# Performance work log

Hardware: AMD Instinct MI355X
Metric: run time of the kernel (lower is better)

## Reference

```python
import jax, jax.numpy as jnp
import numpy as np

N = 100000
E = 1600000
IN_C, HID_C, OUT_C = 128, 64, 40


def setup_inputs() -> dict:
    key = jax.random.key(0)
    ks = jax.random.split(key, 9)
    x = jax.random.normal(ks[0], (N, IN_C), dtype=jnp.float32)
    src = jax.random.randint(ks[1], (E,), 0, N, dtype=jnp.int64)
    dst = jax.random.randint(ks[2], (E,), 0, N, dtype=jnp.int64)
    edge_index = jnp.stack([src, dst], axis=0)
    def glorot(k, fan_in, fan_out):
        s = jnp.sqrt(6.0 / (fan_in + fan_out)).astype(jnp.float32)
        return jax.random.uniform(k, (fan_in, fan_out), jnp.float32, -s, s)
    return {
        "x": x,
        "edge_index": edge_index,
        "W1": glorot(ks[3], IN_C, HID_C), "b1": jnp.zeros((HID_C,), jnp.float32),
        "W2": glorot(ks[4], HID_C, HID_C), "b2": jnp.zeros((HID_C,), jnp.float32),
        "W3": glorot(ks[5], HID_C, OUT_C), "b3": jnp.zeros((OUT_C,), jnp.float32),
    }


def _gcn_norm(edge_index, n_nodes):
    # add self-loops, then symmetric normalization D^-1/2 (A+I) D^-1/2
    loops = jnp.arange(n_nodes, dtype=edge_index.dtype)
    src = jnp.concatenate([edge_index[0], loops])
    dst = jnp.concatenate([edge_index[1], loops])
    deg = jax.ops.segment_sum(jnp.ones_like(dst, dtype=jnp.float32), dst,
                              num_segments=n_nodes)
    dinv = jnp.where(deg > 0, jax.lax.rsqrt(deg), 0.0)
    norm = dinv[src] * dinv[dst]  # [E + N]
    return src, dst, norm


def _gcn_conv(h, W, b, src, dst, norm, n_nodes):
    h = h @ W                                   # [N, out]
    msg = norm[:, None] * h[src]                # gather + scale, [E+N, out]
    out = jax.ops.segment_sum(msg, dst, num_segments=n_nodes)  # scatter-add
    return out + b


def reference(x, edge_index, W1, b1, W2, b2, W3, b3):
    n_nodes = x.shape[0]
    src, dst, norm = _gcn_norm(edge_index, n_nodes)
    h = jax.nn.relu(_gcn_conv(x, W1, b1, src, dst, norm, n_nodes))
    # dropout(p=0.5) is identity in eval mode
    h = jax.nn.relu(_gcn_conv(h, W2, b2, src, dst, norm, n_nodes))
    out = _gcn_conv(h, W3, b3, src, dst, norm, n_nodes)
    return out
```

## Files before the change

### kernel.cpp

```cpp
#include <hip/hip_runtime.h>

#define N_NODES 100000
#define N_EDGES 1600000
#define NBUCK 196
#define BCAP 9600
#define CH 4096
#define NCHUNK ((N_EDGES + CH - 1) / CH)
#define DBINS 64

typedef __attribute__((ext_vector_type(2))) _Float16 half2v;
typedef __attribute__((ext_vector_type(4))) _Float16 half4v;
typedef __attribute__((ext_vector_type(8))) _Float16 half8v;
typedef __attribute__((ext_vector_type(4))) float f32x4;

__device__ __forceinline__ float4 loadX4(const float* X, size_t idx) {
    return *(const float4*)(X + idx);
}
__device__ __forceinline__ float4 loadX4(const _Float16* X, size_t idx) {
    half4v h = *(const half4v*)(X + idx);
    return make_float4((float)h.x, (float)h.y, (float)h.z, (float)h.w);
}


__global__ __launch_bounds__(256) void zero_small(int* p, int n) {
    int i = blockIdx.x * blockDim.x + threadIdx.x;
    if (i < n) p[i] = 0;
}

__global__ __launch_bounds__(256) void multisplit(const int* __restrict__ src,
                                                  const int* __restrict__ dst,
                                                  int* cursor,
                                                  int* __restrict__ bucketed, int e) {
    __shared__ int cnt[NBUCK];
    __shared__ int basel[NBUCK];
    const int t = threadIdx.x;
    const int base_e = blockIdx.x * CH;

    int myS[16], myD[16];
    for (int i = t; i < NBUCK; i += 256) cnt[i] = 0;
    __syncthreads();

#pragma unroll
    for (int k = 0; k < 16; ++k) {
        int i = base_e + k * 256 + t;
        if (i < e) {
            myS[k] = src[i];
            myD[k] = dst[i];
            atomicAdd(&cnt[myD[k] >> 9], 1);
        } else {
            myD[k] = -1;
        }
    }
    __syncthreads();
    for (int i = t; i < NBUCK; i += 256) basel[i] = atomicAdd(&cursor[i], cnt[i]);
    __syncthreads();
    for (int i = t; i < NBUCK; i += 256) cnt[i] = 0;
    __syncthreads();

#pragma unroll
    for (int k = 0; k < 16; ++k) {
        if (myD[k] >= 0) {
            int b = myD[k] >> 9;
            int pos = basel[b] + atomicAdd(&cnt[b], 1);
            if (pos < BCAP)
                bucketed[(size_t)b * BCAP + pos] = ((myD[k] & 511) << 17) | myS[k];
        }
    }
}

__global__ __launch_bounds__(256) void bucket_scan(const int* __restrict__ cursor,
                                                   int* __restrict__ gbase) {
    __shared__ int sm[256];
    const int t = threadIdx.x;
    int v = (t < NBUCK) ? cursor[t] : 0;
    sm[t] = v;
    __syncthreads();
    for (int off = 1; off < 256; off <<= 1) {
        int u = (t >= off) ? sm[t - off] : 0;
        __syncthreads();
        sm[t] += u;
        __syncthreads();
    }
    if (t < NBUCK) gbase[t] = sm[t] - v;
    if (t == NBUCK - 1) gbase[NBUCK] = sm[t];
}

__global__ __launch_bounds__(512) void build_csr(const int* __restrict__ bucketed,
                                                 const int* __restrict__ gbase,
                                                 int* __restrict__ row_ptr,
                                                 float* __restrict__ dinv,
                                                 int* __restrict__ csr_src,
                                                 int* __restrict__ hist, int n) {
    __shared__ int vals[BCAP];
    __shared__ int cnt[512];
    __shared__ int lcur[512];
    __shared__ int lhist[DBINS];
    const int b = blockIdx.x;
    const int t = threadIdx.x;
    const int nb0 = b * 512;
    const int nn = min(512, n - nb0);
    const int gb = gbase[b];
    const int m = gbase[b + 1] - gb;

    cnt[t] = 0;
    if (t < DBINS) lhist[t] = 0;
    __syncthreads();
    for (int i = t; i < m; i += 512) {
        int v = bucketed[(size_t)b * BCAP + i];
        vals[i] = v;
        atomicAdd(&cnt[v >> 17], 1);
    }
    __syncthreads();

    int deg = cnt[t];
    if (t < nn) atomicAdd(&lhist[min(deg, DBINS - 1)], 1);
    for (int off = 1; off < 512; off <<= 1) {
        int u = (t >= off) ? cnt[t - off] : 0;
        __syncthreads();
        cnt[t] += u;
        __syncthreads();
    }
    int offv = cnt[t] - deg;
    __syncthreads();
    cnt[t] = offv;
    lcur[t] = 0;
    if (t < nn) {
        row_ptr[nb0 + t] = gb + offv;
        dinv[nb0 + t] = rsqrtf((float)(deg + 1));
    }
    if (b == NBUCK - 1 && t == 0) row_ptr[n] = gb + m;
    __syncthreads();

    for (int i = t; i < m; i += 512) {
        int v = vals[i];
        int node = v >> 17;
        int pos = atomicAdd(&lcur[node], 1);
        csr_src[gb + cnt[node] + pos] = v & 0x1FFFF;
    }
    if (t < DBINS && lhist[t] > 0) atomicAdd(&hist[t], lhist[t]);
}


__global__ __launch_bounds__(64) void hist_scan(const int* __restrict__ hist,
                                                int* __restrict__ base) {
    __shared__ int sm[DBINS];
    const int t = threadIdx.x;
    int v = hist[t];
    sm[t] = v;
    __syncthreads();
    for (int off = 1; off < DBINS; off <<= 1) {
        int u = (t >= off) ? sm[t - off] : 0;
        __syncthreads();
        sm[t] += u;
        __syncthreads();
    }
    base[t] = sm[t] - v;
}

__global__ __launch_bounds__(256) void perm_scatter(const int* __restrict__ row_ptr,
                                                    const int* __restrict__ base,
                                                    int* gcursor,
                                                    int* __restrict__ perm, int n) {
    __shared__ int lcnt[DBINS];
    __shared__ int lbase[DBINS];
    const int t = threadIdx.x;
    if (t < DBINS) lcnt[t] = 0;
    __syncthreads();
    const int i = blockIdx.x * 256 + t;
    int bin = 0, lpos = 0;
    if (i < n) {
        int deg = row_ptr[i + 1] - row_ptr[i];
        bin = min(deg, DBINS - 1);
        lpos = atomicAdd(&lcnt[bin], 1);
    }
    __syncthreads();
    if (t < DBINS && lcnt[t] > 0) lbase[t] = atomicAdd(&gcursor[t], lcnt[t]);
    __syncthreads();
    if (i < n) perm[base[bin] + lbase[bin] + lpos] = i;
}


template <int K>
__global__ __launch_bounds__(256) void transpose_w(const float* __restrict__ W,
                                                   _Float16* __restrict__ Wt) {
    int i = blockIdx.x * 256 + threadIdx.x;
    if (i < K * 64) {
        int k = i >> 6, nn = i & 63;
        Wt[(size_t)nn * K + k] = (_Float16)W[i];
    }
}


__device__ __forceinline__ void stageX_rows(const float* X, _Float16* Xl, int t,
                                            int row0, int n, int K, int SP) {
    for (int i = t; i < 64 * K / 4; i += 256) {
        int r = i / (K / 4), c = (i % (K / 4)) * 4;
        int grow = min(row0 + r, n - 1);
        float4 v = *(const float4*)(X + (size_t)grow * K + c);
        half4v h = {(_Float16)v.x, (_Float16)v.y, (_Float16)v.z, (_Float16)v.w};
        *(half4v*)(Xl + r * SP + c) = h;
    }
}
__device__ __forceinline__ void stageX_rows(const _Float16* X, _Float16* Xl, int t,
                                            int row0, int n, int K, int SP) {
    for (int i = t; i < 64 * K / 8; i += 256) {
        int r = i / (K / 8), c = (i % (K / 8)) * 8;
        int grow = min(row0 + r, n - 1);
        *(half8v*)(Xl + r * SP + c) = *(const half8v*)(X + (size_t)grow * K + c);
    }
}

template <int K, typename XT>
__global__ __launch_bounds__(256) void gemm_mfma64(const XT* __restrict__ X,
                                                   const _Float16* __restrict__ Wt,
                                                   const float* __restrict__ dinv,
                                                   _Float16* __restrict__ Y, int n) {
    constexpr int SP = K + 8;
    __shared__ _Float16 Xl[64 * SP];
    __shared__ _Float16 Wl[64 * SP];
    const int t = threadIdx.x;
    const int wave = t >> 6, lane = t & 63;
    const int row0 = blockIdx.x * 64;
    const int m = lane & 15, quad = lane >> 4;

    if (blockIdx.x == 0 && t < 32) ((int*)(Y + (size_t)n * 64))[t] = 0;

    for (int i = t; i < 64 * K / 8; i += 256) {
        int r = i / (K / 8), c = (i % (K / 8)) * 8;
        *(half8v*)(Wl + r * SP + c) = *(const half8v*)(Wt + (size_t)r * K + c);
    }
    stageX_rows(X, Xl, t, row0, n, K, SP);
    __syncthreads();

    f32x4 acc[4] = {{0,0,0,0},{0,0,0,0},{0,0,0,0},{0,0,0,0}};
#pragma unroll
    for (int k0 = 0; k0 < K; k0 += 32) {
        half8v a = *(const half8v*)(Xl + (wave * 16 + m) * SP + k0 + quad * 8);
#pragma unroll
        for (int ct = 0; ct < 4; ++ct) {
            half8v b = *(const half8v*)(Wl + (ct * 16 + m) * SP + k0 + quad * 8);
            acc[ct] = __builtin_amdgcn_mfma_f32_16x16x32_f16(a, b, acc[ct], 0, 0, 0);
        }
    }

    float dv[4];
#pragma unroll
    for (int r = 0; r < 4; ++r) {
        int row = row0 + wave * 16 + quad * 4 + r;
        dv[r] = dinv[min(row, n - 1)];
    }
#pragma unroll
    for (int ct = 0; ct < 4; ++ct) {
#pragma unroll
        for (int r = 0; r < 4; ++r) {
            int row = row0 + wave * 16 + quad * 4 + r;
            if (row < n)
                Y[(size_t)row * 64 + ct * 16 + m] = (_Float16)(dv[r] * acc[ct][r]);
        }
    }
}


template <int K, int COUT, typename XT>
__global__ __launch_bounds__(256) void gemm_rt(const XT* __restrict__ X,
                                               const float* __restrict__ W,
                                               const float* __restrict__ dinv,
                                               _Float16* __restrict__ Y, int n) {
    constexpr int KC = 64;
    constexpr int S = KC + 4;
    constexpr int NCH = K / KC;
    __shared__ float Xl[64 * S];
    __shared__ float Wl[KC * COUT];

    const int t = threadIdx.x;
    const int row0 = blockIdx.x * 64;
    const int cg = (t & 15) * 4;
    const int rg = (t >> 4) * 4;

    if (blockIdx.x == 0 && t < COUT / 2) ((int*)(Y + (size_t)n * COUT))[t] = 0;

    float acc[4][4] = {};

#pragma unroll
    for (int ch = 0; ch < NCH; ++ch) {
        const int k0 = ch * KC;
        for (int i = t; i < 64 * KC / 4; i += 256) {
            int r = i >> 4;
            int k = (i & 15) * 4;
            int grow = min(row0 + r, n - 1);
            *(float4*)(Xl + r * S + k) = loadX4(X, (size_t)grow * K + k0 + k);
        }
        for (int i = t; i < KC * COUT / 4; i += 256) {
            *(float4*)(Wl + i * 4) = *(const float4*)(W + (size_t)k0 * COUT + (size_t)i * 4);
        }
        __syncthreads();

        if (cg < COUT) {
#pragma unroll 4
            for (int k = 0; k < KC; ++k) {
                float4 w = *(const float4*)(Wl + k * COUT + cg);
                float x0 = Xl[(rg + 0) * S + k];
                float x1 = Xl[(rg + 1) * S + k];
                float x2 = Xl[(rg + 2) * S + k];
                float x3 = Xl[(rg + 3) * S + k];
                acc[0][0] += x0 * w.x; acc[0][1] += x0 * w.y; acc[0][2] += x0 * w.z; acc[0][3] += x0 * w.w;
                acc[1][0] += x1 * w.x; acc[1][1] += x1 * w.y; acc[1][2] += x1 * w.z; acc[1][3] += x1 * w.w;
                acc[2][0] += x2 * w.x; acc[2][1] += x2 * w.y; acc[2][2] += x2 * w.z; acc[2][3] += x2 * w.w;
                acc[3][0] += x3 * w.x; acc[3][1] += x3 * w.y; acc[3][2] += x3 * w.z; acc[3][3] += x3 * w.w;
            }
        }
        __syncthreads();
    }

    if (cg < COUT) {
#pragma unroll
        for (int r = 0; r < 4; ++r) {
            int row = row0 + rg + r;
            if (row < n) {
                float d = dinv[row];
                half4v o = { (_Float16)(d * acc[r][0]), (_Float16)(d * acc[r][1]),
                             (_Float16)(d * acc[r][2]), (_Float16)(d * acc[r][3]) };
                *(half4v*)(Y + (size_t)row * COUT + cg) = o;
            }
        }
    }
}


template <bool RELU>
__global__ __launch_bounds__(256) void aggregate64g(const _Float16* __restrict__ tS,
                                                    const int* __restrict__ row_ptr,
                                                    const int* __restrict__ csr_src,
                                                    const int* __restrict__ perm,
                                                    const float* __restrict__ dinv,
                                                    const float* __restrict__ bias,
                                                    _Float16* __restrict__ out, int n) {
    const int t = threadIdx.x;
    const int lane = t & 63;
    const int c8 = lane & 7;
    const int node = perm[blockIdx.x * 32 + (t >> 3)];
    const half8v* tS8 = (const half8v*)tS;
    const int bpb = (lane & 56) << 2;

    const int beg = row_ptr[node];
    const int cnt = row_ptr[node + 1] - beg;
    const int cl = (cnt > 0) ? cnt - 1 : 0;

    int mc = cnt;
    mc = max(mc, __shfl_xor(mc, 8));
    mc = max(mc, __shfl_xor(mc, 16));
    mc = max(mc, __shfl_xor(mc, 32));

    half8v acc0, acc1;
#pragma unroll
    for (int i = 0; i < 8; ++i) { acc0[i] = (_Float16)0; acc1[i] = (_Float16)0; }

    for (int j0 = 0; j0 < mc; j0 += 8) {
        int sj = csr_src[beg + min(j0 + c8, cl)];
#pragma unroll
        for (int jj = 0; jj < 8; ++jj) {
            int e = __builtin_amdgcn_ds_bpermute(bpb + jj * 4, sj);
            e = (j0 + jj < cnt) ? e : n;
            half8v v = tS8[(size_t)e * 8 + c8];
            if (jj & 1) acc1 += v; else acc0 += v;
        }
    }

    float acc[8];
#pragma unroll
    for (int i = 0; i < 8; ++i) acc[i] = (float)acc0[i] + (float)acc1[i];

    half8v selfh = tS8[(size_t)node * 8 + c8];
    float4 b0 = ((const float4*)bias)[c8 * 2];
    float4 b1 = ((const float4*)bias)[c8 * 2 + 1];
    const float bb[8] = {b0.x, b0.y, b0.z, b0.w, b1.x, b1.y, b1.z, b1.w};
    float d = dinv[node];
    half8v o;
#pragma unroll
    for (int i = 0; i < 8; ++i) {
        float v = bb[i] + d * (acc[i] + (float)selfh[i]);
        if (RELU) v = fmaxf(v, 0.0f);
        o[i] = (_Float16)v;
    }
    ((half8v*)out)[(size_t)node * 8 + c8] = o;
}


__global__ __launch_bounds__(256) void aggregate40p(const _Float16* __restrict__ tS,
                                                    const int* __restrict__ row_ptr,
                                                    const int* __restrict__ csr_src,
                                                    const int* __restrict__ perm,
                                                    const float* __restrict__ dinv,
                                                    const float* __restrict__ bias,
                                                    float* __restrict__ out, int n) {
    const int t = threadIdx.x;
    const int lane = t & 63;
    const int wave = t >> 6;
    const int g = lane / 5;
    const int c5 = lane - g * 5;
    const int gi = blockIdx.x * 48 + wave * 12 + g;
    const bool act = (g < 12) && (gi < n);
    const int node = act ? perm[gi] : 0;
    const half8v* tS8r = (const half8v*)tS;
    const int bpb = g * 20;

    const int beg = act ? row_ptr[node] : 0;
    const int cnt = act ? (row_ptr[node + 1] - beg) : 0;
    const int cl = (cnt > 0) ? cnt - 1 : 0;

    int mc = cnt;
    mc = max(mc, __shfl_xor(mc, 1));
    mc = max(mc, __shfl_xor(mc, 2));
    mc = max(mc, __shfl_xor(mc, 4));
    mc = max(mc, __shfl_xor(mc, 8));
    mc = max(mc, __shfl_xor(mc, 16));
    mc = max(mc, __shfl_xor(mc, 32));

    half8v a0, a1;
#pragma unroll
    for (int i = 0; i < 8; ++i) { a0[i] = (_Float16)0; a1[i] = (_Float16)0; }

    for (int j0 = 0; j0 < mc; j0 += 5) {
        int sj = csr_src[beg + min(j0 + c5, cl)];
#pragma unroll
        for (int jj = 0; jj < 5; ++jj) {
            int e = __builtin_amdgcn_ds_bpermute(bpb + jj * 4, sj);
            e = (j0 + jj < cnt) ? e : n;
            half8v v = tS8r[(size_t)e * 5 + c5];
            if (jj & 1) a1 += v; else a0 += v;
        }
    }

    if (act) {
        float acc[8];
#pragma unroll
        for (int i = 0; i < 8; ++i) acc[i] = (float)a0[i] + (float)a1[i];

        half8v selfh = tS8r[(size_t)node * 5 + c5];
        float4 b0 = ((const float4*)bias)[c5 * 2];
        float4 b1 = ((const float4*)bias)[c5 * 2 + 1];
        float d = dinv[node];
        float4 o0, o1;
        o0.x = b0.x + d * (acc[0] + (float)selfh[0]);
        o0.y = b0.y + d * (acc[1] + (float)selfh[1]);
        o0.z = b0.z + d * (acc[2] + (float)selfh[2]);
        o0.w = b0.w + d * (acc[3] + (float)selfh[3]);
        o1.x = b1.x + d * (acc[4] + (float)selfh[4]);
        o1.y = b1.y + d * (acc[5] + (float)selfh[5]);
        o1.z = b1.z + d * (acc[6] + (float)selfh[6]);
        o1.w = b1.w + d * (acc[7] + (float)selfh[7]);
        *(float4*)(out + (size_t)node * 40 + c5 * 8) = o0;
        *(float4*)(out + (size_t)node * 40 + c5 * 8 + 4) = o1;
    }
}


extern "C" void kernel_launch(void* const* d_in, const int* in_sizes, int n_in,
                              void* d_out, int out_size, void* d_ws, size_t ws_size,
                              hipStream_t stream) {
    const float* x  = (const float*)d_in[0];
    const int*   ei = (const int*)d_in[1];
    const int*   src = ei;
    const int*   dst = ei + N_EDGES;
    const float* W1 = (const float*)d_in[2];
    const float* b1 = (const float*)d_in[3];
    const float* W2 = (const float*)d_in[4];
    const float* b2 = (const float*)d_in[5];
    const float* W3 = (const float*)d_in[6];
    const float* b3 = (const float*)d_in[7];
    float* out = (float*)d_out;

    const int N = N_NODES, E = N_EDGES;

    char* p = (char*)d_ws;
    int*   cursor   = (int*)p;              p += 256 * 4;
    int*   gbase    = (int*)p;              p += 256 * 4;
    int*   histx    = (int*)p;              p += 256 * 4;
    float* dinv     = (float*)p;            p += (size_t)N * 4;
    int*   row_ptr  = (int*)p;              p += (size_t)(N + 4) * 4;
    int*   perm     = (int*)p;              p += (size_t)N * 4;
    int*   bucketed = (int*)p;              p += (size_t)NBUCK * BCAP * 4;
    int*   csr_src  = (int*)p;              p += (size_t)(E + 64) * 4;
    p = (char*)(((size_t)p + 15) & ~(size_t)15);
    _Float16* Wt1   = (_Float16*)p;         p += (size_t)64 * 128 * 2;
    _Float16* Wt2   = (_Float16*)p;         p += (size_t)64 * 64 * 2;
    _Float16* bufA  = (_Float16*)p;         p += (size_t)(N + 64) * 64 * 2;
    p = (char*)(((size_t)p + 15) & ~(size_t)15);
    _Float16* bufB  = (_Float16*)p;         p += (size_t)N * 64 * 2;

    int* hist    = histx;
    int* gcursor = histx + 64;
    int* dbase   = histx + 128;

    zero_small<<<1, 256, 0, stream>>>(cursor, NBUCK);
    zero_small<<<1, 256, 0, stream>>>(histx, 128);
    transpose_w<128><<<32, 256, 0, stream>>>(W1, Wt1);
    transpose_w<64><<<16, 256, 0, stream>>>(W2, Wt2);
    multisplit<<<NCHUNK, 256, 0, stream>>>(src, dst, cursor, bucketed, E);
    bucket_scan<<<1, 256, 0, stream>>>(cursor, gbase);
    build_csr<<<NBUCK, 512, 0, stream>>>(bucketed, gbase, row_ptr, dinv, csr_src, hist, N);
    hist_scan<<<1, 64, 0, stream>>>(hist, dbase);
    perm_scatter<<<(N + 255) / 256, 256, 0, stream>>>(row_ptr, dbase, gcursor, perm, N);

    const int agg64Grid = N / 32;
    const int agg40Grid = (N + 47) / 48;
    const int gemmGrid = (N + 63) / 64;

    gemm_mfma64<128, float><<<gemmGrid, 256, 0, stream>>>(x, Wt1, dinv, bufA, N);
    aggregate64g<true><<<agg64Grid, 256, 0, stream>>>(bufA, row_ptr, csr_src, perm, dinv, b1, bufB, N);

    gemm_mfma64<64, _Float16><<<gemmGrid, 256, 0, stream>>>(bufB, Wt2, dinv, bufA, N);
    aggregate64g<true><<<agg64Grid, 256, 0, stream>>>(bufA, row_ptr, csr_src, perm, dinv, b2, bufB, N);

    gemm_rt<64, 40, _Float16><<<gemmGrid, 256, 0, stream>>>(bufB, W3, dinv, bufA, N);
    aggregate40p<<<agg40Grid, 256, 0, stream>>>(bufA, row_ptr, csr_src, perm, dinv, b3, out, N);
}
```

Baseline: 345.2 us.

## Renumber nodes by degree order, pad CSR rows, and split aggregation by channel slices

Adds a regroup pass that relabels nodes into degree-sorted order, rewrites the CSR with relabeled sources and rows padded to multiples of eight, and permutes dinv. All intermediate feature buffers are kept in the permuted order, and only the final output is scattered back through perm. The 64-channel aggregation now has each pair of lanes handle one node and a 16-channel slice across four passes, using vectorized int4 index loads. The goal is better gather locality, since each pass touches only a 32-byte slice per neighbor, and less divergence within a wave. The cost is an extra preprocessing kernel and more workspace, plus more index traffic from the padding.

Measured after the change: 584.5 us. +69.3%, slower.

```diff
diff --git a/kernel.cpp b/kernel.cpp
--- a/kernel.cpp
+++ b/kernel.cpp
@@ -141,26 +141,32 @@
 }
 
 
-__global__ __launch_bounds__(64) void hist_scan(const int* __restrict__ hist,
-                                                int* __restrict__ base) {
-    __shared__ int sm[DBINS];
+__global__ __launch_bounds__(64) void hist_scan2(const int* __restrict__ hist,
+                                                 int* __restrict__ dbase,
+                                                 int* __restrict__ ebase) {
+    __shared__ int sa[DBINS];
+    __shared__ int sb[DBINS];
     const int t = threadIdx.x;
     int v = hist[t];
-    sm[t] = v;
+    int w = ((t + 7) & ~7) * v;
+    sa[t] = v; sb[t] = w;
     __syncthreads();
     for (int off = 1; off < DBINS; off <<= 1) {
-        int u = (t >= off) ? sm[t - off] : 0;
-        __syncthreads();
-        sm[t] += u;
-        __syncthreads();
-    }
-    base[t] = sm[t] - v;
+        int ua = (t >= off) ? sa[t - off] : 0;
+        int ub = (t >= off) ? sb[t - off] : 0;
+        __syncthreads();
+        sa[t] += ua; sb[t] += ub;
+        __syncthreads();
+    }
+    dbase[t] = sa[t] - v;
+    ebase[t] = sb[t] - w;
 }
 
 __global__ __launch_bounds__(256) void perm_scatter(const int* __restrict__ row_ptr,
                                                     const int* __restrict__ base,
                                                     int* gcursor,
-                                                    int* __restrict__ perm, int n) {
+                                                    int* __restrict__ perm,
+                                                    int* __restrict__ inv, int n) {
     __shared__ int lcnt[DBINS];
     __shared__ int lbase[DBINS];
     const int t = threadIdx.x;
@@ -176,7 +182,36 @@
     __syncthreads();
     if (t < DBINS && lcnt[t] > 0) lbase[t] = atomicAdd(&gcursor[t], lcnt[t]);
     __syncthreads();
-    if (i < n) perm[base[bin] + lbase[bin] + lpos] = i;
+    if (i < n) {
+        int pos = base[bin] + lbase[bin] + lpos;
+        perm[pos] = i;
+        inv[i] = pos;
+    }
+}
+
+__global__ __launch_bounds__(256) void regroup(const int* __restrict__ row_ptr,
+                                               const int* __restrict__ perm,
+                                               const int* __restrict__ inv,
+                                               const float* __restrict__ dinv,
+                                               const int* __restrict__ dbase,
+                                               const int* __restrict__ ebase,
+                                               const int* __restrict__ csr_src,
+                                               int* __restrict__ csr2,
+                                               int* __restrict__ row_ptr2,
+                                               float* __restrict__ dinv2, int n) {
+    int s = blockIdx.x * 256 + threadIdx.x;
+    if (s >= n) return;
+    int o = perm[s];
+    int beg = row_ptr[o];
+    int deg = row_ptr[o + 1] - beg;
+    int b = min(deg, DBINS - 1);
+    int pdeg = (deg + 7) & ~7;
+    int nb = ebase[b] + (s - dbase[b]) * pdeg;
+    row_ptr2[s] = nb;
+    if (s == n - 1) row_ptr2[n] = nb + pdeg;
+    for (int j = 0; j < deg; ++j) csr2[nb + j] = inv[csr_src[beg + j]];
+    for (int j = deg; j < pdeg; ++j) csr2[nb + j] = n;
+    dinv2[s] = dinv[o];
 }
 
 
@@ -192,20 +227,24 @@
 
 
 __device__ __forceinline__ void stageX_rows(const float* X, _Float16* Xl, int t,
-                                            int row0, int n, int K, int SP) {
+                                            int row0, int n, int K, int SP,
+                                            const int* perm) {
     for (int i = t; i < 64 * K / 4; i += 256) {
         int r = i / (K / 4), c = (i % (K / 4)) * 4;
         int grow = min(row0 + r, n - 1);
+        if (perm) grow = perm[grow];
         float4 v = *(const float4*)(X + (size_t)grow * K + c);
         half4v h = {(_Float16)v.x, (_Float16)v.y, (_Float16)v.z, (_Float16)v.w};
         *(half4v*)(Xl + r * SP + c) = h;
     }
 }
 __device__ __forceinline__ void stageX_rows(const _Float16* X, _Float16* Xl, int t,
-                                            int row0, int n, int K, int SP) {
+                                            int row0, int n, int K, int SP,
+                                            const int* perm) {
     for (int i = t; i < 64 * K / 8; i += 256) {
         int r = i / (K / 8), c = (i % (K / 8)) * 8;
         int grow = min(row0 + r, n - 1);
+        if (perm) grow = perm[grow];
         *(half8v*)(Xl + r * SP + c) = *(const half8v*)(X + (size_t)grow * K + c);
     }
 }
@@ -213,7 +252,8 @@
 template <int K, typename XT>
 __global__ __launch_bounds__(256) void gemm_mfma64(const XT* __restrict__ X,
                                                    const _Float16* __restrict__ Wt,
-                                                   const float* __restrict__ dinv,
+                                                   const float* __restrict__ dinv2,
+                                                   const int* __restrict__ perm,
                                                    _Float16* __restrict__ Y, int n) {
     constexpr int SP = K + 8;
     __shared__ _Float16 Xl[64 * SP];
@@ -229,7 +269,7 @@
         int r = i / (K / 8), c = (i % (K / 8)) * 8;
         *(half8v*)(Wl + r * SP + c) = *(const half8v*)(Wt + (size_t)r * K + c);
     }
-    stageX_rows(X, Xl, t, row0, n, K, SP);
+    stageX_rows(X, Xl, t, row0, n, K, SP, perm);
     __syncthreads();
 
     f32x4 acc[4] = {{0,0,0,0},{0,0,0,0},{0,0,0,0},{0,0,0,0}};
@@ -247,7 +287,7 @@
 #pragma unroll
     for (int r = 0; r < 4; ++r) {
         int row = row0 + wave * 16 + quad * 4 + r;
-        dv[r] = dinv[min(row, n - 1)];
+        dv[r] = dinv2[min(row, n - 1)];
     }
 #pragma unroll
     for (int ct = 0; ct < 4; ++ct) {
@@ -264,7 +304,7 @@
 template <int K, int COUT, typename XT>
 __global__ __launch_bounds__(256) void gemm_rt(const XT* __restrict__ X,
                                                const float* __restrict__ W,
-                                               const float* __restrict__ dinv,
+                                               const float* __restrict__ dinv2,
                                                _Float16* __restrict__ Y, int n) {
     constexpr int KC = 64;
     constexpr int S = KC + 4;
@@ -317,7 +357,7 @@
         for (int r = 0; r < 4; ++r) {
             int row = row0 + rg + r;
             if (row < n) {
-                float d = dinv[row];
+                float d = dinv2[row];
                 half4v o = { (_Float16)(d * acc[r][0]), (_Float16)(d * acc[r][1]),
                              (_Float16)(d * acc[r][2]), (_Float16)(d * acc[r][3]) };
                 *(half4v*)(Y + (size_t)row * COUT + cg) = o;
@@ -328,53 +368,60 @@
 
 
 template <bool RELU>
-__global__ __launch_bounds__(256) void aggregate64g(const _Float16* __restrict__ tS,
-                                                    const int* __restrict__ row_ptr,
-                                                    const int* __restrict__ csr_src,
-                                                    const int* __restrict__ perm,
-                                                    const float* __restrict__ dinv,
-                                                    const float* __restrict__ bias,
-                                                    _Float16* __restrict__ out, int n) {
+__global__ __launch_bounds__(256) void aggregate64cs(const _Float16* __restrict__ tS,
+                                                     const int* __restrict__ row_ptr2,
+                                                     const int* __restrict__ csr2,
+                                                     const float* __restrict__ dinv2,
+                                                     const float* __restrict__ bias,
+                                                     _Float16* __restrict__ out, int n) {
     const int t = threadIdx.x;
     const int lane = t & 63;
-    const int c8 = lane & 7;
-    const int node = perm[blockIdx.x * 32 + (t >> 3)];
-    const half8v* tS8 = (const half8v*)tS;
-    const int bpb = (lane & 56) << 2;
-
-    const int beg = row_ptr[node];
-    const int cnt = row_ptr[node + 1] - beg;
-    const int cl = (cnt > 0) ? cnt - 1 : 0;
-
-    int mc = cnt;
+    const int c2 = lane & 1;
+    const int bid = blockIdx.x;
+    const int pass = (bid & 7) >> 1;
+    const int chunk = (bid >> 3) * 2 + (bid & 1);
+    const int s = min(chunk * 128 + (t >> 1), n - 1);
+    const int bpb = (lane & 62) << 2;
+    const int ch0 = pass * 16 + c2 * 8;
+
+    const int beg = row_ptr2[s];
+    const int pcnt = row_ptr2[s + 1] - beg;
+
+    int mc = pcnt;
+    mc = max(mc, __shfl_xor(mc, 2));
+    mc = max(mc, __shfl_xor(mc, 4));
     mc = max(mc, __shfl_xor(mc, 8));
     mc = max(mc, __shfl_xor(mc, 16));
     mc = max(mc, __shfl_xor(mc, 32));
 
-    half8v acc0, acc1;
-#pragma unroll
-    for (int i = 0; i < 8; ++i) { acc0[i] = (_Float16)0; acc1[i] = (_Float16)0; }
-
+    half8v a0, a1;
+#pragma unroll
+    for (int i = 0; i < 8; ++i) { a0[i] = (_Float16)0; a1[i] = (_Float16)0; }
+
+    const _Float16* tbase = tS + ch0;
     for (int j0 = 0; j0 < mc; j0 += 8) {
-        int sj = csr_src[beg + min(j0 + c8, cl)];
-#pragma unroll
-        for (int jj = 0; jj < 8; ++jj) {
-            int e = __builtin_amdgcn_ds_bpermute(bpb + jj * 4, sj);
-            e = (j0 + jj < cnt) ? e : n;
-            half8v v = tS8[(size_t)e * 8 + c8];
-            if (jj & 1) acc1 += v; else acc0 += v;
+        int j0c = min(j0, max(pcnt - 8, 0));
+        int4 sj = *(const int4*)(csr2 + beg + j0c + c2 * 4);
+#pragma unroll
+        for (int k = 0; k < 8; ++k) {
+            int srcv = ((k & 3) == 0) ? sj.x : ((k & 3) == 1) ? sj.y
+                     : ((k & 3) == 2) ? sj.z : sj.w;
+            int e = __builtin_amdgcn_ds_bpermute(bpb + (k >> 2) * 4, srcv);
+            e = (j0 + k < pcnt) ? e : n;
+            half8v v = *(const half8v*)(tbase + (size_t)e * 64);
+            if (k & 1) a1 += v; else a0 += v;
         }
     }
 
     float acc[8];
 #pragma unroll
-    for (int i = 0; i < 8; ++i) acc[i] = (float)acc0[i] + (float)acc1[i];
-
-    half8v selfh = tS8[(size_t)node * 8 + c8];
-    float4 b0 = ((const float4*)bias)[c8 * 2];
-    float4 b1 = ((const float4*)bias)[c8 * 2 + 1];
+    for (int i = 0; i < 8; ++i) acc[i] = (float)a0[i] + (float)a1[i];
+
+    half8v selfh = *(const half8v*)(tS + (size_t)s * 64 + ch0);
+    float4 b0 = *(const float4*)(bias + ch0);
+    float4 b1 = *(const float4*)(bias + ch0 + 4);
     const float bb[8] = {b0.x, b0.y, b0.z, b0.w, b1.x, b1.y, b1.z, b1.w};
-    float d = dinv[node];
+    float d = dinv2[s];
     half8v o;
 #pragma unroll
     for (int i = 0; i < 8; ++i) {
@@ -382,30 +429,30 @@
         if (RELU) v = fmaxf(v, 0.0f);
         o[i] = (_Float16)v;
     }
-    ((half8v*)out)[(size_t)node * 8 + c8] = o;
-}
-
-
-__global__ __launch_bounds__(256) void aggregate40p(const _Float16* __restrict__ tS,
-                                                    const int* __restrict__ row_ptr,
-                                                    const int* __restrict__ csr_src,
+    *(half8v*)(out + (size_t)s * 64 + ch0) = o;
+}
+
+
+__global__ __launch_bounds__(256) void aggregate40s(const _Float16* __restrict__ tS,
+                                                    const int* __restrict__ row_ptr2,
+                                                    const int* __restrict__ csr2,
+                                                    const float* __restrict__ dinv2,
                                                     const int* __restrict__ perm,
-                                                    const float* __restrict__ dinv,
                                                     const float* __restrict__ bias,
                                                     float* __restrict__ out, int n) {
     const int t = threadIdx.x;
     const int lane = t & 63;
     const int wave = t >> 6;
-    const int g = lane / 5;
-    const int c5 = lane - g * 5;
-    const int gi = blockIdx.x * 48 + wave * 12 + g;
-    const bool act = (g < 12) && (gi < n);
-    const int node = act ? perm[gi] : 0;
-    const half8v* tS8r = (const half8v*)tS;
-    const int bpb = g * 20;
-
-    const int beg = act ? row_ptr[node] : 0;
-    const int cnt = act ? (row_ptr[node + 1] - beg) : 0;
+    const int g = lane / 10;
+    const int c10 = lane - g * 10;
+    const int s = blockIdx.x * 24 + wave * 6 + g;
+    const bool act = (g < 6) && (s < n);
+    const half4v* tS4 = (const half4v*)tS;
+    const int bpb = g * 40;
+
+    const int sc = act ? s : 0;
+    const int beg = row_ptr2[sc];
+    const int cnt = act ? (row_ptr2[sc + 1] - beg) : 0;
     const int cl = (cnt > 0) ? cnt - 1 : 0;
 
     int mc = cnt;
@@ -416,41 +463,36 @@
     mc = max(mc, __shfl_xor(mc, 16));
     mc = max(mc, __shfl_xor(mc, 32));
 
-    half8v a0, a1;
-#pragma unroll
-    for (int i = 0; i < 8; ++i) { a0[i] = (_Float16)0; a1[i] = (_Float16)0; }
-
-    for (int j0 = 0; j0 < mc; j0 += 5) {
-        int sj = csr_src[beg + min(j0 + c5, cl)];
-#pragma unroll
-        for (int jj = 0; jj < 5; ++jj) {
+    half4v a0, a1;
+#pragma unroll
+    for (int i = 0; i < 4; ++i) { a0[i] = (_Float16)0; a1[i] = (_Float16)0; }
+
+    for (int j0 = 0; j0 < mc; j0 += 10) {
+        int sj = csr2[beg + min(j0 + c10, cl)];
+#pragma unroll
+        for (int jj = 0; jj < 10; ++jj) {
             int e = __builtin_amdgcn_ds_bpermute(bpb + jj * 4, sj);
             e = (j0 + jj < cnt) ? e : n;
-            half8v v = tS8r[(size_t)e * 5 + c5];
+            half4v v = tS4[(size_t)e * 10 + c10];
             if (jj & 1) a1 += v; else a0 += v;
         }
     }
 
     if (act) {
-        float acc[8];
-#pragma unroll
-        for (int i = 0; i < 8; ++i) acc[i] = (float)a0[i] + (float)a1[i];
-
-        half8v selfh = tS8r[(size_t)node * 5 + c5];
-        float4 b0 = ((const float4*)bias)[c5 * 2];
-        float4 b1 = ((const float4*)bias)[c5 * 2 + 1];
-        float d = dinv[node];
-        float4 o0, o1;
-        o0.x = b0.x + d * (acc[0] + (float)selfh[0]);
-        o0.y = b0.y + d * (acc[1] + (float)selfh[1]);
-        o0.z = b0.z + d * (acc[2] + (float)selfh[2]);
-        o0.w = b0.w + d * (acc[3] + (float)selfh[3]);
-        o1.x = b1.x + d * (acc[4] + (float)selfh[4]);
-        o1.y = b1.y + d * (acc[5] + (float)selfh[5]);
-        o1.z = b1.z + d * (acc[6] + (float)selfh[6]);
-        o1.w = b1.w + d * (acc[7] + (float)selfh[7]);
-        *(float4*)(out + (size_t)node * 40 + c5 * 8) = o0;
-        *(float4*)(out + (size_t)node * 40 + c5 * 8 + 4) = o1;
+        float acc[4];
+#pragma unroll
+        for (int i = 0; i < 4; ++i) acc[i] = (float)a0[i] + (float)a1[i];
+
+        half4v selfh = tS4[(size_t)s * 10 + c10];
+        float4 b = ((const float4*)bias)[c10];
+        float d = dinv2[s];
+        int orow = perm[s];
+        float4 o;
+        o.x = b.x + d * (acc[0] + (float)selfh[0]);
+        o.y = b.y + d * (acc[1] + (float)selfh[1]);
+        o.z = b.z + d * (acc[2] + (float)selfh[2]);
+        o.w = b.w + d * (acc[3] + (float)selfh[3]);
+        *(float4*)(out + (size_t)orow * 40 + c10 * 4) = o;
     }
 }
 
@@ -477,10 +519,14 @@
     int*   gbase    = (int*)p;              p += 256 * 4;
     int*   histx    = (int*)p;              p += 256 * 4;
     float* dinv     = (float*)p;            p += (size_t)N * 4;
+    float* dinv2    = (float*)p;            p += (size_t)N * 4;
     int*   row_ptr  = (int*)p;              p += (size_t)(N + 4) * 4;
+    int*   row_ptr2 = (int*)p;              p += (size_t)(N + 8) * 4;
     int*   perm     = (int*)p;              p += (size_t)N * 4;
+    int*   inv      = (int*)p;              p += (size_t)N * 4;
     int*   bucketed = (int*)p;              p += (size_t)NBUCK * BCAP * 4;
     int*   csr_src  = (int*)p;              p += (size_t)(E + 64) * 4;
+    int*   csr2     = (int*)p;              p += ((size_t)E + 8 * (size_t)N + 64) * 4;
     p = (char*)(((size_t)p + 15) & ~(size_t)15);
     _Float16* Wt1   = (_Float16*)p;         p += (size_t)64 * 128 * 2;
     _Float16* Wt2   = (_Float16*)p;         p += (size_t)64 * 64 * 2;
@@ -491,6 +537,7 @@
     int* hist    = histx;
     int* gcursor = histx + 64;
     int* dbase   = histx + 128;
+    int* ebase   = histx + 192;
 
     zero_small<<<1, 256, 0, stream>>>(cursor, NBUCK);
     zero_small<<<1, 256, 0, stream>>>(histx, 128);
@@ -499,19 +546,21 @@
     multisplit<<<NCHUNK, 256, 0, stream>>>(src, dst, cursor, bucketed, E);
     bucket_scan<<<1, 256, 0, stream>>>(cursor, gbase);
     build_csr<<<NBUCK, 512, 0, stream>>>(bucketed, gbase, row_ptr, dinv, csr_src, hist, N);
-    hist_scan<<<1, 64, 0, stream>>>(hist, dbase);
-    perm_scatter<<<(N + 255) / 256, 256, 0, stream>>>(row_ptr, dbase, gcursor, perm, N);
-
-    const int agg64Grid = N / 32;
-    const int agg40Grid = (N + 47) / 48;
+    hist_scan2<<<1, 64, 0, stream>>>(hist, dbase, ebase);
+    perm_scatter<<<(N + 255) / 256, 256, 0, stream>>>(row_ptr, dbase, gcursor, perm, inv, N);
+    regroup<<<(N + 255) / 256, 256, 0, stream>>>(row_ptr, perm, inv, dinv, dbase, ebase,
+                                                 csr_src, csr2, row_ptr2, dinv2, N);
+
     const int gemmGrid = (N + 63) / 64;
-
-    gemm_mfma64<128, float><<<gemmGrid, 256, 0, stream>>>(x, Wt1, dinv, bufA, N);
-    aggregate64g<true><<<agg64Grid, 256, 0, stream>>>(bufA, row_ptr, csr_src, perm, dinv, b1, bufB, N);
-
-    gemm_mfma64<64, _Float16><<<gemmGrid, 256, 0, stream>>>(bufB, Wt2, dinv, bufA, N);
-    aggregate64g<true><<<agg64Grid, 256, 0, stream>>>(bufA, row_ptr, csr_src, perm, dinv, b2, bufB, N);
-
-    gemm_rt<64, 40, _Float16><<<gemmGrid, 256, 0, stream>>>(bufB, W3, dinv, bufA, N);
-    aggregate40p<<<agg40Grid, 256, 0, stream>>>(bufA, row_ptr, csr_src, perm, dinv, b3, out, N);
-}
+    const int aggcsGrid = 8 * (((N + 127) / 128 + 1) / 2);
+    const int agg40Grid = (N + 23) / 24;
+
+    gemm_mfma64<128, float><<<gemmGrid, 256, 0, stream>>>(x, Wt1, dinv2, perm, bufA, N);
+    aggregate64cs<true><<<aggcsGrid, 256, 0, stream>>>(bufA, row_ptr2, csr2, dinv2, b1, bufB, N);
+
+    gemm_mfma64<64, _Float16><<<gemmGrid, 256, 0, stream>>>(bufB, Wt2, dinv2, nullptr, bufA, N);
+    aggregate64cs<true><<<aggcsGrid, 256, 0, stream>>>(bufA, row_ptr2, csr2, dinv2, b2, bufB, N);
+
+    gemm_rt<64, 40, _Float16><<<gemmGrid, 256, 0, stream>>>(bufB, W3, dinv2, bufA, N);
+    aggregate40s<<<agg40Grid, 256, 0, stream>>>(bufA, row_ptr2, csr2, dinv2, perm, b3, out, N);
+}
```
